# Kernel tuning notes

Measured on AMD Instinct MI355X. Metric: run time of the kernel, lower is better.

## Reference

```python
import jax, jax.numpy as jnp
import numpy as np

N, E = 50000, 800000
F_IN, HID, HEADS, OUT, NG = 128, 32, 4, 64, 64
HD = HID * HEADS  # 128


def gat_layer(x, src, dst, W, a_s, a_d, b, heads, out_c):
    n = x.shape[0]
    h = (x @ W).reshape(n, heads, out_c)                      # [N,H,C]
    al_s = jnp.einsum('nhc,hc->nh', h, a_s)                   # [N,H]
    al_d = jnp.einsum('nhc,hc->nh', h, a_d)
    e = jax.nn.leaky_relu(al_s[src] + al_d[dst], 0.2)         # [E,H]
    m = jax.ops.segment_max(e, dst, num_segments=n)
    ex = jnp.exp(e - m[dst])
    s = jax.ops.segment_sum(ex, dst, num_segments=n)
    alpha = ex / (s[dst] + 1e-16)                             # [E,H]
    msg = h[src] * alpha[:, :, None]                          # [E,H,C]
    out = jax.ops.segment_sum(msg, dst, num_segments=n)       # [N,H,C]
    return out.reshape(n, heads * out_c) + b


def batchnorm(x, g, be, eps=1e-5):
    mu = x.mean(0)
    var = x.var(0)
    return (x - mu) * jax.lax.rsqrt(var + eps) * g + be


def setup_inputs():
    key = jax.random.key(0)
    ks = jax.random.split(key, 32)
    inp = {}
    inp['x'] = jax.random.normal(ks[0], (N, F_IN), dtype=jnp.float32)
    inp['edge_index'] = jax.random.randint(ks[1], (2, E), 0, N, dtype=jnp.int64)
    inp['batch_ids'] = jnp.sort(jax.random.randint(ks[2], (N,), 0, NG, dtype=jnp.int64))
    dims = [(F_IN, HEADS, HID), (HD, HEADS, HID), (HD, HEADS, HID), (HD, 1, OUT)]
    for i, (din, h, c) in enumerate(dims):
        sc = 1.0 / np.sqrt(din)
        inp[f'W{i}'] = jax.random.normal(ks[3 + 4 * i], (din, h * c), dtype=jnp.float32) * sc
        inp[f'as{i}'] = jax.random.normal(ks[4 + 4 * i], (h, c), dtype=jnp.float32) * 0.1
        inp[f'ad{i}'] = jax.random.normal(ks[5 + 4 * i], (h, c), dtype=jnp.float32) * 0.1
        inp[f'b{i}'] = jnp.zeros((h * c,), dtype=jnp.float32)
    for i in range(3):
        inp[f'g{i}'] = jnp.ones((HD,), dtype=jnp.float32)
        inp[f'be{i}'] = jnp.zeros((HD,), dtype=jnp.float32)
    return inp


def reference(x, edge_index, batch_ids,
              W0, as0, ad0, b0, W1, as1, ad1, b1,
              W2, as2, ad2, b2, W3, as3, ad3, b3,
              g0, be0, g1, be1, g2, be2):
    # add self-loops (PyG GATConv default)
    loop = jnp.arange(N, dtype=edge_index.dtype)
    src = jnp.concatenate([edge_index[0], loop])
    dst = jnp.concatenate([edge_index[1], loop])

    h = x
    layers = [(W0, as0, ad0, b0, g0, be0), (W1, as1, ad1, b1, g1, be1),
              (W2, as2, ad2, b2, g2, be2)]
    for (W, a_s, a_d, b, g, be) in layers:
        h = gat_layer(h, src, dst, W, a_s, a_d, b, HEADS, HID)
        h = jax.nn.elu(batchnorm(h, g, be))
        # dropout p=0.6 is identity at inference
    h = gat_layer(h, src, dst, W3, as3, ad3, b3, 1, OUT)     # [N,OUT]

    # global mean pool over graphs
    ones = jnp.ones((N,), dtype=h.dtype)
    cnt = jax.ops.segment_sum(ones, batch_ids, num_segments=NG)
    summed = jax.ops.segment_sum(h, batch_ids, num_segments=NG)
    return summed / jnp.maximum(cnt, 1.0)[:, None]           # [NG,OUT]
```

## Files before the change

### kernel.cpp

```cpp
#include <hip/hip_runtime.h>

#define DEVINL __device__ __forceinline__

constexpr int N_NODES = 50000;
constexpr int E_EDGES = 800000;
constexpr int HD      = 128;
constexpr int NG      = 64;
constexpr int OUTC    = 64;
constexpr int NPAR    = 22;
constexpr int PAR_TOTAL = 3*(16384+3*128) + (8192+3*64) + 6*128;
constexpr int WT_TOTAL = 3*128*128 + 64*128;
constexpr int NB      = (N_NODES + 1023) / 1024;
constexpr int EBC     = 2048;
constexpr int NBLKC   = (E_EDGES + EBC - 1) / EBC;
constexpr int BNSLOTS = 16;

typedef _Float16 half8_t __attribute__((ext_vector_type(8)));
typedef _Float16 half4_t __attribute__((ext_vector_type(4)));
typedef float    float4_t __attribute__((ext_vector_type(4)));

DEVINL float bf2f(unsigned short u){
  union { unsigned int i; float f; } v; v.i = ((unsigned int)u) << 16; return v.f;
}
DEVINL float lrelu(float v){ return v > 0.f ? v : 0.2f * v; }

struct PtrTab { const void* p[NPAR]; int off[NPAR + 1]; };

__global__ void k_prep(PtrTab tab, const unsigned short* __restrict__ x,
                       const int* __restrict__ ei, int* __restrict__ flags,
                       float* __restrict__ dst,
                       const void* __restrict__ W0, const void* __restrict__ W1,
                       const void* __restrict__ W2, const void* __restrict__ W3,
                       _Float16* __restrict__ wt16){
  __shared__ int s_f32, s_i64;
  int t = threadIdx.x;
  if (t == 0){ s_f32 = 0; s_i64 = 1; }
  __syncthreads();
  for (int i = t; i < 2048; i += 256){
    float v = bf2f(x[i]);
    if (!(fabsf(v) < 1e4f)) s_f32 = 1;
  }
  for (int i = t; i < 512; i += 256){
    if (ei[2 * i + 1] != 0) s_i64 = 0;
  }
  __syncthreads();
  int f = s_f32;
  if (blockIdx.x == 0 && t == 0){ flags[0] = s_i64; flags[1] = s_f32; }

  int i = blockIdx.x * 256 + t;
  if (i < PAR_TOTAL){
    int k = 0;
    while (tab.off[k + 1] <= i) k++;
    int j = i - tab.off[k];
    dst[i] = f ? ((const float*)tab.p[k])[j] : bf2f(((const unsigned short*)tab.p[k])[j]);
    return;
  }
  int w = i - PAR_TOTAL;
  if (w >= WT_TOTAL) return;
  const void* W; int base, Mt;
  if (w < 49152){ int l = w >> 14; base = w & 16383; Mt = 128; W = (l == 0) ? W0 : (l == 1 ? W1 : W2); }
  else { base = w - 49152; Mt = 64; W = W3; }
  int nn = base >> 7, k = base & 127;
  float val = f ? ((const float*)W)[(size_t)k * Mt + nn]
                : bf2f(((const unsigned short*)W)[(size_t)k * Mt + nn]);
  wt16[w] = (_Float16)val;
}

__global__ __launch_bounds__(256) void k_count(const int* __restrict__ ei,
                      const int* __restrict__ flags, int* __restrict__ cntmat){
  __shared__ int cnt[NB];
  int t = threadIdx.x, blk = blockIdx.x;
  if (t < NB) cnt[t] = 0;
  __syncthreads();
  int f = flags[0];
  int e0 = blk * EBC;
  #pragma unroll
  for (int j = 0; j < EBC / 256; j++){
    int e = e0 + t + j * 256;
    if (e < E_EDGES){
      int d = ei[(size_t)(E_EDGES + e) << f];
      atomicAdd(&cnt[d >> 10], 1);
    }
  }
  __syncthreads();
  if (t < NB) cntmat[blk * NB + t] = cnt[t];
}

__global__ void k_scanmat(const int* __restrict__ cntmat, int* __restrict__ gbase,
                          int* __restrict__ bbase){
  __shared__ int cbase[NB + 1];
  __shared__ int csum[NB];
  int t = threadIdx.x;
  int s = 0;
  if (t < NB){
    for (int blk = 0; blk < NBLKC; blk++) s += cntmat[blk * NB + t];
    csum[t] = s;
  }
  __syncthreads();
  if (t == 0){
    int run = 0;
    for (int b = 0; b < NB; b++){ cbase[b] = run; run += csum[b]; }
    cbase[NB] = run;
  }
  __syncthreads();
  if (t <= NB) bbase[t] = cbase[t];
  if (t < NB){
    int run = cbase[t];
    for (int blk = 0; blk < NBLKC; blk++){
      gbase[blk * NB + t] = run;
      run += cntmat[blk * NB + t];
    }
  }
}

__global__ __launch_bounds__(256) void k_binscatter(const int* __restrict__ ei,
                      const int* __restrict__ flags, const int* __restrict__ gbase,
                      unsigned int* __restrict__ ebuf2){
  __shared__ int cur[NB];
  int t = threadIdx.x, blk = blockIdx.x;
  if (t < NB) cur[t] = gbase[blk * NB + t];
  __syncthreads();
  int f = flags[0];
  int e0 = blk * EBC;
  #pragma unroll
  for (int j = 0; j < EBC / 256; j++){
    int e = e0 + t + j * 256;
    if (e < E_EDGES){
      int s = ei[(size_t)e << f];
      int d = ei[(size_t)(E_EDGES + e) << f];
      int p = atomicAdd(&cur[d >> 10], 1);
      ebuf2[p] = (unsigned int)s | ((unsigned int)d << 16);
    }
  }
}

__global__ __launch_bounds__(256) void k_csrD(const unsigned int* __restrict__ ebuf2,
                      const int* __restrict__ bbase, int* __restrict__ offs,
                      int* __restrict__ ssrc, int n){
  __shared__ int hist[1024];
  __shared__ int wsum[256];
  int t = threadIdx.x, b = blockIdx.x;
  int nbase = b << 10;
  int s0 = bbase[b], s1 = bbase[b + 1];
  for (int i = t; i < 1024; i += 256) hist[i] = 0;
  __syncthreads();
  for (int i = s0 + t; i < s1; i += 256){
    unsigned int pk = ebuf2[i];
    atomicAdd(&hist[(int)(pk >> 16) - nbase], 1);
  }
  __syncthreads();
  int base4 = t * 4;
  int v0 = hist[base4], v1 = hist[base4 + 1], v2 = hist[base4 + 2], v3 = hist[base4 + 3];
  int s = v0 + v1 + v2 + v3;
  wsum[t] = s; __syncthreads();
  for (int off = 1; off < 256; off <<= 1){
    int x2 = (t >= off) ? wsum[t - off] : 0;
    __syncthreads();
    wsum[t] += x2;
    __syncthreads();
  }
  int run = s0 + wsum[t] - s;
  int node = nbase + base4;
  if (node < n) offs[node] = run;  hist[base4] = run;  run += v0;
  if (node + 1 < n) offs[node + 1] = run;  hist[base4 + 1] = run;  run += v1;
  if (node + 2 < n) offs[node + 2] = run;  hist[base4 + 2] = run;  run += v2;
  if (node + 3 < n) offs[node + 3] = run;  hist[base4 + 3] = run;
  if (b == NB - 1 && t == 255) offs[n] = s1;
  __syncthreads();
  for (int i = s0 + t; i < s1; i += 256){
    unsigned int pk = ebuf2[i];
    int p = atomicAdd(&hist[(int)(pk >> 16) - nbase], 1);
    ssrc[p] = (int)(pk & 0xFFFFu);
  }
}

template<int MT, bool FIRST>
__global__ __launch_bounds__(256) void k_gemm(
    const void* __restrict__ Ain, const int* __restrict__ flags,
    const float* __restrict__ bnslots,
    const float* __restrict__ g, const float* __restrict__ be,
    const _Float16* __restrict__ Wt16,
    const float* __restrict__ a_s, const float* __restrict__ a_d,
    _Float16* __restrict__ h16, float* __restrict__ als, float* __restrict__ ald,
    int n){
  __shared__ _Float16 AhL[64 * 136];
  __shared__ _Float16 WtL[MT * 72];
  __shared__ float scale[128], shift[128];
  const int t = threadIdx.x;
  const int rowBase = blockIdx.x * 64;
  if (!FIRST){
    if (t < 128){
      float s = 0.f, q = 0.f;
      #pragma unroll
      for (int sl = 0; sl < BNSLOTS; sl++){
        s += bnslots[sl * 256 + t];
        q += bnslots[sl * 256 + 128 + t];
      }
      float inv_n = 1.f / (float)n;
      float mu = s * inv_n;
      float var = q * inv_n - mu * mu;
      float sc = g[t] * rsqrtf(var + 1e-5f);
      scale[t] = sc; shift[t] = be[t] - mu * sc;
    }
    __syncthreads();
  }
  for (int f = t; f < 64 * 16; f += 256){
    int r = f >> 4, c8 = (f & 15) << 3;
    int row = rowBase + r;
    float v[8];
    if (row < n){
      if (FIRST){
        if (flags[1]){
          float4 x0 = *(const float4*)((const float*)Ain + (size_t)row * 128 + c8);
          float4 x1 = *(const float4*)((const float*)Ain + (size_t)row * 128 + c8 + 4);
          v[0]=x0.x; v[1]=x0.y; v[2]=x0.z; v[3]=x0.w;
          v[4]=x1.x; v[5]=x1.y; v[6]=x1.z; v[7]=x1.w;
        } else {
          const unsigned short* xp = (const unsigned short*)Ain + (size_t)row * 128 + c8;
          ushort4 u0 = *(const ushort4*)xp; ushort4 u1 = *(const ushort4*)(xp + 4);
          v[0]=bf2f(u0.x); v[1]=bf2f(u0.y); v[2]=bf2f(u0.z); v[3]=bf2f(u0.w);
          v[4]=bf2f(u1.x); v[5]=bf2f(u1.y); v[6]=bf2f(u1.z); v[7]=bf2f(u1.w);
        }
      } else {
        half8_t a8 = *(const half8_t*)((const _Float16*)Ain + (size_t)row * 128 + c8);
        #pragma unroll
        for (int j = 0; j < 8; j++){
          float xv = (float)a8[j] * scale[c8 + j] + shift[c8 + j];
          v[j] = xv > 0.f ? xv : (__expf(xv) - 1.f);
        }
      }
    } else {
      #pragma unroll
      for (int j = 0; j < 8; j++) v[j] = 0.f;
    }
    half8_t h;
    #pragma unroll
    for (int j = 0; j < 8; j++) h[j] = (_Float16)v[j];
    *(half8_t*)&AhL[r * 136 + c8] = h;
  }
  const int lane = t & 63;
  const int m = lane & 15, quad = lane >> 4;
  const int band = (t >> 6) * 16;
  float4_t acc[MT / 16];
  #pragma unroll
  for (int ct = 0; ct < MT / 16; ct++) acc[ct] = (float4_t){0.f, 0.f, 0.f, 0.f};
  #pragma unroll
  for (int kh = 0; kh < 2; kh++){
    __syncthreads();
    for (int f = t; f < MT * 8; f += 256){
      int nn = f >> 3, c8 = (f & 7) << 3;
      *(half8_t*)&WtL[nn * 72 + c8] = *(const half8_t*)&Wt16[nn * 128 + kh * 64 + c8];
    }
    __syncthreads();
    half8_t a0 = *(half8_t*)&AhL[(band + m) * 136 + kh * 64 + quad * 8];
    half8_t a1 = *(half8_t*)&AhL[(band + m) * 136 + kh * 64 + 32 + quad * 8];
    #pragma unroll
    for (int ct = 0; ct < MT / 16; ct++){
      half8_t b0 = *(half8_t*)&WtL[(ct * 16 + m) * 72 + quad * 8];
      half8_t b1 = *(half8_t*)&WtL[(ct * 16 + m) * 72 + 32 + quad * 8];
      acc[ct] = __builtin_amdgcn_mfma_f32_16x16x32_f16(a0, b0, acc[ct], 0, 0, 0);
      acc[ct] = __builtin_amdgcn_mfma_f32_16x16x32_f16(a1, b1, acc[ct], 0, 0, 0);
    }
  }
  __syncthreads();
  #pragma unroll
  for (int ct = 0; ct < MT / 16; ct++)
    #pragma unroll
    for (int rg = 0; rg < 4; rg++)
      AhL[(band + quad * 4 + rg) * 136 + ct * 16 + m] = (_Float16)acc[ct][rg];
  __syncthreads();
  int r = t >> 2, q = t & 3;
  int row = rowBase + r;
  if (MT == 128){
    if (row < n){
      half8_t h0 = *(half8_t*)&AhL[r * 136 + q * 32];
      half8_t h1 = *(half8_t*)&AhL[r * 136 + q * 32 + 8];
      half8_t h2 = *(half8_t*)&AhL[r * 136 + q * 32 + 16];
      half8_t h3 = *(half8_t*)&AhL[r * 136 + q * 32 + 24];
      float pas = 0.f, pad = 0.f;
      #pragma unroll
      for (int j = 0; j < 8; j++){
        pas += (float)h0[j] * a_s[q * 32 + j]      + (float)h1[j] * a_s[q * 32 + 8 + j]
             + (float)h2[j] * a_s[q * 32 + 16 + j] + (float)h3[j] * a_s[q * 32 + 24 + j];
        pad += (float)h0[j] * a_d[q * 32 + j]      + (float)h1[j] * a_d[q * 32 + 8 + j]
             + (float)h2[j] * a_d[q * 32 + 16 + j] + (float)h3[j] * a_d[q * 32 + 24 + j];
      }
      als[(size_t)row * 4 + q] = pas;
      ald[(size_t)row * 4 + q] = pad;
      _Float16* hp = h16 + (size_t)row * 128 + q * 32;
      *(half8_t*)hp = h0; *(half8_t*)(hp + 8) = h1;
      *(half8_t*)(hp + 16) = h2; *(half8_t*)(hp + 24) = h3;
    }
  } else {
    half8_t h0 = *(half8_t*)&AhL[r * 136 + q * 16];
    half8_t h1 = *(half8_t*)&AhL[r * 136 + q * 16 + 8];
    float pas = 0.f, pad = 0.f;
    #pragma unroll
    for (int j = 0; j < 8; j++){
      pas += (float)h0[j] * a_s[q * 16 + j] + (float)h1[j] * a_s[q * 16 + 8 + j];
      pad += (float)h0[j] * a_d[q * 16 + j] + (float)h1[j] * a_d[q * 16 + 8 + j];
    }
    pas += __shfl_xor(pas, 1); pas += __shfl_xor(pas, 2);
    pad += __shfl_xor(pad, 1); pad += __shfl_xor(pad, 2);
    if (row < n){
      _Float16* hp = h16 + (size_t)row * 64 + q * 16;
      *(half8_t*)hp = h0; *(half8_t*)(hp + 8) = h1;
      if (q == 0){ als[row] = pas; ald[row] = pad; }
    }
  }
}

template<int H, int C, int MODE>
__global__ __launch_bounds__(256) void k_attn(const _Float16* __restrict__ h16,
                      const float* __restrict__ als, const float* __restrict__ ald,
                      const int* __restrict__ offs, const int* __restrict__ ssrc,
                      const float* __restrict__ bias,
                      _Float16* __restrict__ a16out, float* __restrict__ bnout,
                      const int* __restrict__ bids, const int* __restrict__ flags,
                      float* __restrict__ psum, int* __restrict__ gcnt, int n){
  constexpr int HC = H * C;
  constexpr int CPL = HC / 16;
  int t = threadIdx.x;
  int nib  = t >> 4;
  int node = blockIdx.x * 16 + nib;
  int sub  = t & 15;
  int c0   = sub * CPL;
  int head = c0 / C;

  float ald_h = ald[(size_t)node * H + head];
  float acc[CPL];
  float ssum;
  {
    float w = __expf(lrelu(als[(size_t)node * H + head] + ald_h));
    ssum = w;
    const _Float16* hp = h16 + (size_t)node * HC + c0;
    #pragma unroll
    for (int i = 0; i < CPL; i++) acc[i] = w * (float)hp[i];
  }
  int beg = offs[node];
  int deg = offs[node + 1] - beg;
  int j = 0;
  for (; j + 8 <= deg; j += 8){
    int ss[8]; float al[8]; float w[8];
    #pragma unroll
    for (int u = 0; u < 8; u++) ss[u] = ssrc[beg + j + u];
    #pragma unroll
    for (int u = 0; u < 8; u++) al[u] = als[(size_t)ss[u] * H + head];
    if constexpr (CPL == 8){
      half8_t v[8];
      #pragma unroll
      for (int u = 0; u < 8; u++) v[u] = *(const half8_t*)(h16 + (size_t)ss[u] * HC + c0);
      #pragma unroll
      for (int u = 0; u < 8; u++){ w[u] = __expf(lrelu(al[u] + ald_h)); ssum += w[u]; }
      #pragma unroll
      for (int i = 0; i < 8; i++){
        float a = 0.f;
        #pragma unroll
        for (int u = 0; u < 8; u++) a += w[u] * (float)v[u][i];
        acc[i] += a;
      }
    } else {
      half4_t v[8];
      #pragma unroll
      for (int u = 0; u < 8; u++) v[u] = *(const half4_t*)(h16 + (size_t)ss[u] * HC + c0);
      #pragma unroll
      for (int u = 0; u < 8; u++){ w[u] = __expf(lrelu(al[u] + ald_h)); ssum += w[u]; }
      #pragma unroll
      for (int i = 0; i < 4; i++){
        float a = 0.f;
        #pragma unroll
        for (int u = 0; u < 8; u++) a += w[u] * (float)v[u][i];
        acc[i] += a;
      }
    }
  }
  for (; j + 4 <= deg; j += 4){
    int s0 = ssrc[beg + j], s1 = ssrc[beg + j + 1];
    int s2 = ssrc[beg + j + 2], s3 = ssrc[beg + j + 3];
    float al0 = als[(size_t)s0 * H + head], al1 = als[(size_t)s1 * H + head];
    float al2 = als[(size_t)s2 * H + head], al3 = als[(size_t)s3 * H + head];
    float w0 = __expf(lrelu(al0 + ald_h)), w1 = __expf(lrelu(al1 + ald_h));
    float w2 = __expf(lrelu(al2 + ald_h)), w3 = __expf(lrelu(al3 + ald_h));
    ssum += (w0 + w1) + (w2 + w3);
    if constexpr (CPL == 8){
      half8_t v0 = *(const half8_t*)(h16 + (size_t)s0 * HC + c0);
      half8_t v1 = *(const half8_t*)(h16 + (size_t)s1 * HC + c0);
      half8_t v2 = *(const half8_t*)(h16 + (size_t)s2 * HC + c0);
      half8_t v3 = *(const half8_t*)(h16 + (size_t)s3 * HC + c0);
      #pragma unroll
      for (int i = 0; i < 8; i++)
        acc[i] += w0 * (float)v0[i] + w1 * (float)v1[i]
                + w2 * (float)v2[i] + w3 * (float)v3[i];
    } else {
      half4_t v0 = *(const half4_t*)(h16 + (size_t)s0 * HC + c0);
      half4_t v1 = *(const half4_t*)(h16 + (size_t)s1 * HC + c0);
      half4_t v2 = *(const half4_t*)(h16 + (size_t)s2 * HC + c0);
      half4_t v3 = *(const half4_t*)(h16 + (size_t)s3 * HC + c0);
      #pragma unroll
      for (int i = 0; i < 4; i++)
        acc[i] += w0 * (float)v0[i] + w1 * (float)v1[i]
                + w2 * (float)v2[i] + w3 * (float)v3[i];
    }
  }
  for (; j < deg; j++){
    int s0 = ssrc[beg + j];
    float w0 = __expf(lrelu(als[(size_t)s0 * H + head] + ald_h));
    ssum += w0;
    const _Float16* hp = h16 + (size_t)s0 * HC + c0;
    #pragma unroll
    for (int i = 0; i < CPL; i++) acc[i] += w0 * (float)hp[i];
  }
  float inv_s = 1.f / ssum;
  float v[CPL];
  #pragma unroll
  for (int i = 0; i < CPL; i++) v[i] = acc[i] * inv_s + bias[c0 + i];

  if constexpr (MODE == 0){
    _Float16* op = a16out + (size_t)node * HC + c0;
    half8_t o;
    #pragma unroll
    for (int i = 0; i < CPL; i++) o[i] = (_Float16)v[i];
    *(half8_t*)op = o;
    __shared__ float red[16][132];
    *(float4*)&red[nib][c0]     = make_float4(v[0], v[1], v[2], v[3]);
    *(float4*)&red[nib][c0 + 4] = make_float4(v[4], v[5], v[6], v[7]);
    __syncthreads();
    if (t < 128){
      float s = 0.f, q = 0.f;
      #pragma unroll
      for (int i = 0; i < 16; i++){ float x = red[i][t]; s += x; q += x * x; }
      int slot = blockIdx.x & (BNSLOTS - 1);
      atomicAdd(&bnout[slot * 256 + t], s);
      atomicAdd(&bnout[slot * 256 + 128 + t], q);
    }
  } else {
    __shared__ float pacc[2][64];
    __shared__ int pcnt[2];
    int f = flags[0];
    if (t < 128) pacc[t >> 6][t & 63] = 0.f;
    if (t < 2) pcnt[t] = 0;
    __syncthreads();
    int g  = (int)bids[(size_t)node << f];
    int g0 = (int)bids[(size_t)(blockIdx.x * 16) << f];
    int g1 = (int)bids[(size_t)(blockIdx.x * 16 + 15) << f];
    if (g1 - g0 <= 1){
      int gl = g - g0;
      #pragma unroll
      for (int i = 0; i < 4; i++) atomicAdd(&pacc[gl][c0 + i], v[i]);
      if (sub == 0) atomicAdd(&pcnt[gl], 1);
      __syncthreads();
      if (t < 128){
        int gl2 = t >> 6;
        if (pcnt[gl2] > 0) atomicAdd(&psum[(g0 + gl2) * 64 + (t & 63)], pacc[gl2][t & 63]);
      }
      if (t < 2 && pcnt[t] > 0) atomicAdd(&gcnt[g0 + t], pcnt[t]);
    } else {
      #pragma unroll
      for (int i = 0; i < 4; i++) atomicAdd(&psum[g * 64 + c0 + i], v[i]);
      if (sub == 0) atomicAdd(&gcnt[g], 1);
      __syncthreads();
    }
  }
}

__global__ void k_pool_fin(const float* __restrict__ psum, const int* __restrict__ gcnt,
                           float* __restrict__ out){
  int i = blockIdx.x * 256 + threadIdx.x;
  if (i >= NG * OUTC) return;
  int cnt = gcnt[i >> 6];
  out[i] = psum[i] / (float)(cnt > 1 ? cnt : 1);
}

extern "C" void kernel_launch(void* const* d_in, const int* in_sizes, int n_in,
                              void* d_out, int out_size, void* d_ws, size_t ws_size,
                              hipStream_t stream){
  const unsigned short* x    = (const unsigned short*)d_in[0];
  const int*            ei   = (const int*)d_in[1];
  const int*            bids = (const int*)d_in[2];

  char* p = (char*)d_ws;
  auto carve = [&](size_t bytes) -> void* {
    void* r = (void*)p; p += (bytes + 255) & ~size_t(255); return r;
  };
  _Float16* a16    = (_Float16*)carve((size_t)N_NODES * HD * 2);
  _Float16* h16    = (_Float16*)carve((size_t)N_NODES * HD * 2);
  float*    par    = (float*)carve((size_t)PAR_TOTAL * 4);
  _Float16* wt16   = (_Float16*)carve((size_t)WT_TOTAL * 2);
  float*    als    = (float*)carve((size_t)N_NODES * 4 * 4);
  float*    ald    = (float*)carve((size_t)N_NODES * 4 * 4);
  int*      offs   = (int*)carve((size_t)(N_NODES + 1) * 4);
  int*      ssrc   = (int*)carve((size_t)E_EDGES * 4);
  unsigned int* ebuf2 = (unsigned int*)carve((size_t)E_EDGES * 4);
  int*      cntmat = (int*)carve((size_t)NBLKC * NB * 4);
  int*      gbase  = (int*)carve((size_t)NBLKC * NB * 4);
  int*      bbase  = (int*)carve((size_t)(NB + 1) * 4);
  int*      flags  = (int*)carve(256);
  char*     zbeg   = p;
  float*    bnbuf  = (float*)carve((size_t)3 * BNSLOTS * 256 * 4);
  float*    psum   = (float*)carve(NG * OUTC * 4);
  int*      gcnt   = (int*)carve(256);
  size_t    zlen   = (size_t)(p - zbeg);

  PtrTab tab;
  int sizes[NPAR];
  for (int l = 0; l < 4; l++){
    int base = 3 + 4 * l;
    tab.p[4 * l + 0] = d_in[base + 0]; sizes[4 * l + 0] = (l < 3) ? 16384 : 8192;
    tab.p[4 * l + 1] = d_in[base + 1]; sizes[4 * l + 1] = (l < 3) ? 128 : 64;
    tab.p[4 * l + 2] = d_in[base + 2]; sizes[4 * l + 2] = (l < 3) ? 128 : 64;
    tab.p[4 * l + 3] = d_in[base + 3]; sizes[4 * l + 3] = (l < 3) ? 128 : 64;
  }
  for (int l = 0; l < 3; l++){
    tab.p[16 + 2 * l]     = d_in[19 + 2 * l];     sizes[16 + 2 * l] = 128;
    tab.p[16 + 2 * l + 1] = d_in[19 + 2 * l + 1]; sizes[16 + 2 * l + 1] = 128;
  }
  tab.off[0] = 0;
  for (int k = 0; k < NPAR; k++) tab.off[k + 1] = tab.off[k] + sizes[k];
  const float* pAS[4], *pAD[4], *pB[4], *pG[3], *pBE[3];
  for (int l = 0; l < 4; l++){
    pAS[l] = par + tab.off[4 * l + 1];
    pAD[l] = par + tab.off[4 * l + 2];
    pB[l]  = par + tab.off[4 * l + 3];
  }
  for (int l = 0; l < 3; l++){
    pG[l]  = par + tab.off[16 + 2 * l];
    pBE[l] = par + tab.off[16 + 2 * l + 1];
  }
  const _Float16* pWT[4] = { wt16, wt16 + 16384, wt16 + 32768, wt16 + 49152 };
  float* bnS[3];
  for (int l = 0; l < 3; l++) bnS[l] = bnbuf + (size_t)l * BNSLOTS * 256;

  hipMemsetAsync(zbeg, 0, zlen, stream);

  k_prep<<<(PAR_TOTAL + WT_TOTAL + 255) / 256, 256, 0, stream>>>(
      tab, x, ei, flags, par, d_in[3], d_in[7], d_in[11], d_in[15], wt16);

  k_count<<<NBLKC, 256, 0, stream>>>(ei, flags, cntmat);
  k_scanmat<<<1, 256, 0, stream>>>(cntmat, gbase, bbase);
  k_binscatter<<<NBLKC, 256, 0, stream>>>(ei, flags, gbase, ebuf2);
  k_csrD<<<NB, 256, 0, stream>>>(ebuf2, bbase, offs, ssrc, N_NODES);

  int gemmBlocks = (N_NODES + 63) / 64;
  int attnBlocks = N_NODES / 16;

  k_gemm<128, true><<<gemmBlocks, 256, 0, stream>>>(
      (const void*)x, flags, nullptr, nullptr, nullptr,
      pWT[0], pAS[0], pAD[0], h16, als, ald, N_NODES);
  k_attn<4, 32, 0><<<attnBlocks, 256, 0, stream>>>(h16, als, ald, offs, ssrc, pB[0],
      a16, bnS[0], nullptr, nullptr, nullptr, nullptr, N_NODES);
  for (int l = 1; l < 3; l++){
    k_gemm<128, false><<<gemmBlocks, 256, 0, stream>>>(
        (const void*)a16, flags, bnS[l-1], pG[l-1], pBE[l-1],
        pWT[l], pAS[l], pAD[l], h16, als, ald, N_NODES);
    k_attn<4, 32, 0><<<attnBlocks, 256, 0, stream>>>(h16, als, ald, offs, ssrc, pB[l],
        a16, bnS[l], nullptr, nullptr, nullptr, nullptr, N_NODES);
  }
  k_gemm<64, false><<<gemmBlocks, 256, 0, stream>>>(
      (const void*)a16, flags, bnS[2], pG[2], pBE[2],
      pWT[3], pAS[3], pAD[3], h16, als, ald, N_NODES);
  k_attn<1, 64, 1><<<attnBlocks, 256, 0, stream>>>(h16, als, ald, offs, ssrc, pB[3],
      nullptr, nullptr, bids, flags, psum, gcnt, N_NODES);

  k_pool_fin<<<16, 256, 0, stream>>>(psum, gcnt, (float*)d_out);
}
```

Before: 437.1 us.

## Fuse CSR build kernels into one cooperative kernel with grid syncs

Merges the prep, count, scan, bin-scatter and CSR kernels into a single cooperative launch separated by grid-wide barriers. Packed edges are kept in registers between the count and scatter phases, so the edge list is read only once. The count matrix is transposed so that a parallel per-bin scan replaces the single-block serial scan. This removes several launch gaps and a second read of the edges, at the cost of grid.sync overhead and a hard requirement that all NBLKC blocks be co-resident.

New measurement: 632.9 us. 44.8% more time.

```diff
diff --git a/kernel.cpp b/kernel.cpp
--- a/kernel.cpp
+++ b/kernel.cpp
@@ -1,4 +1,7 @@
 #include <hip/hip_runtime.h>
+#include <hip/hip_cooperative_groups.h>
+
+namespace cg = cooperative_groups;
 
 #define DEVINL __device__ __forceinline__
 
@@ -26,14 +29,22 @@
 
 struct PtrTab { const void* p[NPAR]; int off[NPAR + 1]; };
 
-__global__ void k_prep(PtrTab tab, const unsigned short* __restrict__ x,
-                       const int* __restrict__ ei, int* __restrict__ flags,
-                       float* __restrict__ dst,
-                       const void* __restrict__ W0, const void* __restrict__ W1,
-                       const void* __restrict__ W2, const void* __restrict__ W3,
-                       _Float16* __restrict__ wt16){
+__global__ __launch_bounds__(256) void k_build(PtrTab tab,
+    const unsigned short* __restrict__ x, const int* __restrict__ ei,
+    int* __restrict__ flags, float* __restrict__ par,
+    const void* __restrict__ W0, const void* __restrict__ W1,
+    const void* __restrict__ W2, const void* __restrict__ W3,
+    _Float16* __restrict__ wt16,
+    int* __restrict__ cntmat,
+    int* __restrict__ gbase,
+    int* __restrict__ csum_g,
+    int* __restrict__ cbase,
+    unsigned int* __restrict__ ebuf2,
+    int* __restrict__ offs, int* __restrict__ ssrc){
+  cg::grid_group grid = cg::this_grid();
+  int t = threadIdx.x, blk = blockIdx.x;
+
   __shared__ int s_f32, s_i64;
-  int t = threadIdx.x;
   if (t == 0){ s_f32 = 0; s_i64 = 1; }
   __syncthreads();
   for (int i = t; i < 2048; i += 256){
@@ -44,133 +55,120 @@
     if (ei[2 * i + 1] != 0) s_i64 = 0;
   }
   __syncthreads();
-  int f = s_f32;
-  if (blockIdx.x == 0 && t == 0){ flags[0] = s_i64; flags[1] = s_f32; }
-
-  int i = blockIdx.x * 256 + t;
-  if (i < PAR_TOTAL){
-    int k = 0;
-    while (tab.off[k + 1] <= i) k++;
-    int j = i - tab.off[k];
-    dst[i] = f ? ((const float*)tab.p[k])[j] : bf2f(((const unsigned short*)tab.p[k])[j]);
-    return;
-  }
-  int w = i - PAR_TOTAL;
-  if (w >= WT_TOTAL) return;
-  const void* W; int base, Mt;
-  if (w < 49152){ int l = w >> 14; base = w & 16383; Mt = 128; W = (l == 0) ? W0 : (l == 1 ? W1 : W2); }
-  else { base = w - 49152; Mt = 64; W = W3; }
-  int nn = base >> 7, k = base & 127;
-  float val = f ? ((const float*)W)[(size_t)k * Mt + nn]
-                : bf2f(((const unsigned short*)W)[(size_t)k * Mt + nn]);
-  wt16[w] = (_Float16)val;
-}
-
-__global__ __launch_bounds__(256) void k_count(const int* __restrict__ ei,
-                      const int* __restrict__ flags, int* __restrict__ cntmat){
+  const int f32 = s_f32, i64 = s_i64;
+  if (blk == 0 && t == 0){ flags[0] = i64; flags[1] = f32; }
+
+  for (int i = blk * 256 + t; i < PAR_TOTAL + WT_TOTAL; i += gridDim.x * 256){
+    if (i < PAR_TOTAL){
+      int k = 0;
+      while (tab.off[k + 1] <= i) k++;
+      int j = i - tab.off[k];
+      par[i] = f32 ? ((const float*)tab.p[k])[j] : bf2f(((const unsigned short*)tab.p[k])[j]);
+    } else {
+      int w = i - PAR_TOTAL;
+      const void* W; int base, Mt;
+      if (w < 49152){ int l = w >> 14; base = w & 16383; Mt = 128; W = (l == 0) ? W0 : (l == 1 ? W1 : W2); }
+      else { base = w - 49152; Mt = 64; W = W3; }
+      int nn = base >> 7, k = base & 127;
+      float val = f32 ? ((const float*)W)[(size_t)k * Mt + nn]
+                      : bf2f(((const unsigned short*)W)[(size_t)k * Mt + nn]);
+      wt16[w] = (_Float16)val;
+    }
+  }
+
+  unsigned int my[EBC / 256];
   __shared__ int cnt[NB];
-  int t = threadIdx.x, blk = blockIdx.x;
-  if (t < NB) cnt[t] = 0;
-  __syncthreads();
-  int f = flags[0];
-  int e0 = blk * EBC;
-  #pragma unroll
-  for (int j = 0; j < EBC / 256; j++){
-    int e = e0 + t + j * 256;
-    if (e < E_EDGES){
-      int d = ei[(size_t)(E_EDGES + e) << f];
-      atomicAdd(&cnt[d >> 10], 1);
-    }
-  }
-  __syncthreads();
-  if (t < NB) cntmat[blk * NB + t] = cnt[t];
-}
-
-__global__ void k_scanmat(const int* __restrict__ cntmat, int* __restrict__ gbase,
-                          int* __restrict__ bbase){
-  __shared__ int cbase[NB + 1];
-  __shared__ int csum[NB];
-  int t = threadIdx.x;
-  int s = 0;
-  if (t < NB){
-    for (int blk = 0; blk < NBLKC; blk++) s += cntmat[blk * NB + t];
-    csum[t] = s;
-  }
-  __syncthreads();
-  if (t == 0){
+  if (blk < NBLKC){
+    if (t < NB) cnt[t] = 0;
+    __syncthreads();
+    int e0 = blk * EBC;
+    #pragma unroll
+    for (int j = 0; j < EBC / 256; j++){
+      int e = e0 + t + j * 256;
+      my[j] = 0xFFFFFFFFu;
+      if (e < E_EDGES){
+        int s = ei[(size_t)e << i64];
+        int d = ei[(size_t)(E_EDGES + e) << i64];
+        my[j] = (unsigned int)s | ((unsigned int)d << 16);
+        atomicAdd(&cnt[d >> 10], 1);
+      }
+    }
+    __syncthreads();
+    if (t < NB) cntmat[t * NBLKC + blk] = cnt[t];
+  }
+  grid.sync();
+
+  __shared__ int vals[NBLKC];
+  if (blk < NB){
+    for (int k = t; k < NBLKC; k += 256) vals[k] = cntmat[blk * NBLKC + k];
+    __syncthreads();
+    if (t == 0){
+      int run = 0;
+      for (int k = 0; k < NBLKC; k++){ int c = vals[k]; vals[k] = run; run += c; }
+      csum_g[blk] = run;
+    }
+    __syncthreads();
+    for (int k = t; k < NBLKC; k += 256) gbase[blk * NBLKC + k] = vals[k];
+  }
+  grid.sync();
+
+  if (blk == 0 && t == 0){
     int run = 0;
-    for (int b = 0; b < NB; b++){ cbase[b] = run; run += csum[b]; }
+    for (int b = 0; b < NB; b++){ cbase[b] = run; run += csum_g[b]; }
     cbase[NB] = run;
   }
-  __syncthreads();
-  if (t <= NB) bbase[t] = cbase[t];
-  if (t < NB){
-    int run = cbase[t];
-    for (int blk = 0; blk < NBLKC; blk++){
-      gbase[blk * NB + t] = run;
-      run += cntmat[blk * NB + t];
-    }
-  }
-}
-
-__global__ __launch_bounds__(256) void k_binscatter(const int* __restrict__ ei,
-                      const int* __restrict__ flags, const int* __restrict__ gbase,
-                      unsigned int* __restrict__ ebuf2){
+  grid.sync();
+
   __shared__ int cur[NB];
-  int t = threadIdx.x, blk = blockIdx.x;
-  if (t < NB) cur[t] = gbase[blk * NB + t];
-  __syncthreads();
-  int f = flags[0];
-  int e0 = blk * EBC;
-  #pragma unroll
-  for (int j = 0; j < EBC / 256; j++){
-    int e = e0 + t + j * 256;
-    if (e < E_EDGES){
-      int s = ei[(size_t)e << f];
-      int d = ei[(size_t)(E_EDGES + e) << f];
-      int p = atomicAdd(&cur[d >> 10], 1);
-      ebuf2[p] = (unsigned int)s | ((unsigned int)d << 16);
-    }
-  }
-}
-
-__global__ __launch_bounds__(256) void k_csrD(const unsigned int* __restrict__ ebuf2,
-                      const int* __restrict__ bbase, int* __restrict__ offs,
-                      int* __restrict__ ssrc, int n){
+  if (blk < NBLKC){
+    if (t < NB) cur[t] = gbase[t * NBLKC + blk] + cbase[t];
+    __syncthreads();
+    #pragma unroll
+    for (int j = 0; j < EBC / 256; j++){
+      unsigned int pk = my[j];
+      if (pk != 0xFFFFFFFFu){
+        int p = atomicAdd(&cur[pk >> 26], 1);
+        ebuf2[p] = pk;
+      }
+    }
+  }
+  grid.sync();
+
   __shared__ int hist[1024];
   __shared__ int wsum[256];
-  int t = threadIdx.x, b = blockIdx.x;
-  int nbase = b << 10;
-  int s0 = bbase[b], s1 = bbase[b + 1];
-  for (int i = t; i < 1024; i += 256) hist[i] = 0;
-  __syncthreads();
-  for (int i = s0 + t; i < s1; i += 256){
-    unsigned int pk = ebuf2[i];
-    atomicAdd(&hist[(int)(pk >> 16) - nbase], 1);
-  }
-  __syncthreads();
-  int base4 = t * 4;
-  int v0 = hist[base4], v1 = hist[base4 + 1], v2 = hist[base4 + 2], v3 = hist[base4 + 3];
-  int s = v0 + v1 + v2 + v3;
-  wsum[t] = s; __syncthreads();
-  for (int off = 1; off < 256; off <<= 1){
-    int x2 = (t >= off) ? wsum[t - off] : 0;
-    __syncthreads();
-    wsum[t] += x2;
-    __syncthreads();
-  }
-  int run = s0 + wsum[t] - s;
-  int node = nbase + base4;
-  if (node < n) offs[node] = run;  hist[base4] = run;  run += v0;
-  if (node + 1 < n) offs[node + 1] = run;  hist[base4 + 1] = run;  run += v1;
-  if (node + 2 < n) offs[node + 2] = run;  hist[base4 + 2] = run;  run += v2;
-  if (node + 3 < n) offs[node + 3] = run;  hist[base4 + 3] = run;
-  if (b == NB - 1 && t == 255) offs[n] = s1;
-  __syncthreads();
-  for (int i = s0 + t; i < s1; i += 256){
-    unsigned int pk = ebuf2[i];
-    int p = atomicAdd(&hist[(int)(pk >> 16) - nbase], 1);
-    ssrc[p] = (int)(pk & 0xFFFFu);
+  if (blk < NB){
+    int nbase = blk << 10;
+    int s0 = cbase[blk], s1 = cbase[blk + 1];
+    for (int i = t; i < 1024; i += 256) hist[i] = 0;
+    __syncthreads();
+    for (int i = s0 + t; i < s1; i += 256){
+      unsigned int pk = ebuf2[i];
+      atomicAdd(&hist[(int)(pk >> 16) - nbase], 1);
+    }
+    __syncthreads();
+    int base4 = t * 4;
+    int v0 = hist[base4], v1 = hist[base4 + 1], v2 = hist[base4 + 2], v3 = hist[base4 + 3];
+    int s = v0 + v1 + v2 + v3;
+    wsum[t] = s; __syncthreads();
+    for (int off = 1; off < 256; off <<= 1){
+      int x2 = (t >= off) ? wsum[t - off] : 0;
+      __syncthreads();
+      wsum[t] += x2;
+      __syncthreads();
+    }
+    int run = s0 + wsum[t] - s;
+    int node = nbase + base4;
+    if (node < N_NODES) offs[node] = run;  hist[base4] = run;  run += v0;
+    if (node + 1 < N_NODES) offs[node + 1] = run;  hist[base4 + 1] = run;  run += v1;
+    if (node + 2 < N_NODES) offs[node + 2] = run;  hist[base4 + 2] = run;  run += v2;
+    if (node + 3 < N_NODES) offs[node + 3] = run;  hist[base4 + 3] = run;
+    if (blk == NB - 1 && t == 255) offs[N_NODES] = s1;
+    __syncthreads();
+    for (int i = s0 + t; i < s1; i += 256){
+      unsigned int pk = ebuf2[i];
+      int p = atomicAdd(&hist[(int)(pk >> 16) - nbase], 1);
+      ssrc[p] = (int)(pk & 0xFFFFu);
+    }
   }
 }
 
@@ -491,9 +489,10 @@
   int*      offs   = (int*)carve((size_t)(N_NODES + 1) * 4);
   int*      ssrc   = (int*)carve((size_t)E_EDGES * 4);
   unsigned int* ebuf2 = (unsigned int*)carve((size_t)E_EDGES * 4);
-  int*      cntmat = (int*)carve((size_t)NBLKC * NB * 4);
-  int*      gbase  = (int*)carve((size_t)NBLKC * NB * 4);
-  int*      bbase  = (int*)carve((size_t)(NB + 1) * 4);
+  int*      cntmat = (int*)carve((size_t)NB * NBLKC * 4);
+  int*      gbase  = (int*)carve((size_t)NB * NBLKC * 4);
+  int*      csum_g = (int*)carve(256);
+  int*      cbase  = (int*)carve((size_t)(NB + 1) * 4);
   int*      flags  = (int*)carve(256);
   char*     zbeg   = p;
   float*    bnbuf  = (float*)carve((size_t)3 * BNSLOTS * 256 * 4);
@@ -532,13 +531,12 @@
 
   hipMemsetAsync(zbeg, 0, zlen, stream);
 
-  k_prep<<<(PAR_TOTAL + WT_TOTAL + 255) / 256, 256, 0, stream>>>(
-      tab, x, ei, flags, par, d_in[3], d_in[7], d_in[11], d_in[15], wt16);
-
-  k_count<<<NBLKC, 256, 0, stream>>>(ei, flags, cntmat);
-  k_scanmat<<<1, 256, 0, stream>>>(cntmat, gbase, bbase);
-  k_binscatter<<<NBLKC, 256, 0, stream>>>(ei, flags, gbase, ebuf2);
-  k_csrD<<<NB, 256, 0, stream>>>(ebuf2, bbase, offs, ssrc, N_NODES);
+  const void* W0 = d_in[3], *W1 = d_in[7], *W2 = d_in[11], *W3 = d_in[15];
+  void* args[] = { (void*)&tab, (void*)&x, (void*)&ei, (void*)&flags, (void*)&par,
+                   (void*)&W0, (void*)&W1, (void*)&W2, (void*)&W3, (void*)&wt16,
+                   (void*)&cntmat, (void*)&gbase, (void*)&csum_g, (void*)&cbase,
+                   (void*)&ebuf2, (void*)&offs, (void*)&ssrc };
+  hipLaunchCooperativeKernel((void*)k_build, dim3(NBLKC), dim3(256), args, 0, stream);
 
   int gemmBlocks = (N_NODES + 63) / 64;
   int attnBlocks = N_NODES / 16;
```

## Replace per-block count matrix scan with global atomic bin totals and cursors

Applied to the files above, without the earlier changes.

The per-block bin count matrix and its serial single-block scan are replaced by global atomic per-bin totals, a tiny prefix kernel, and atomic cursor reservation inside the scatter kernel. This removes the sequential loop over about 400 blocks per bin in the scan kernel, which was a serial bottleneck. The scatter kernel now keeps packed edges in registers and does a local histogram before reserving global ranges, so edge order within a bin becomes nondeterministic. The CSR build kernel sorts by destination within each bin, so correctness is preserved, though source order per node may vary.

Result: faster. 422.9 us (-3.2%).

```diff
diff --git a/kernel.cpp b/kernel.cpp
--- a/kernel.cpp
+++ b/kernel.cpp
@@ -67,7 +67,7 @@
 }
 
 __global__ __launch_bounds__(256) void k_count(const int* __restrict__ ei,
-                      const int* __restrict__ flags, int* __restrict__ cntmat){
+                      const int* __restrict__ flags, int* __restrict__ btot){
   __shared__ int cnt[NB];
   int t = threadIdx.x, blk = blockIdx.x;
   if (t < NB) cnt[t] = 0;
@@ -83,65 +83,66 @@
     }
   }
   __syncthreads();
-  if (t < NB) cntmat[blk * NB + t] = cnt[t];
-}
-
-__global__ void k_scanmat(const int* __restrict__ cntmat, int* __restrict__ gbase,
-                          int* __restrict__ bbase){
-  __shared__ int cbase[NB + 1];
-  __shared__ int csum[NB];
+  if (t < NB && cnt[t] > 0) atomicAdd(&btot[t], cnt[t]);
+}
+
+__global__ void k_cbase(const int* __restrict__ btot, int* __restrict__ cbase,
+                        int* __restrict__ cursor){
   int t = threadIdx.x;
-  int s = 0;
-  if (t < NB){
-    for (int blk = 0; blk < NBLKC; blk++) s += cntmat[blk * NB + t];
-    csum[t] = s;
-  }
-  __syncthreads();
+  __shared__ int cb[NB + 1];
   if (t == 0){
     int run = 0;
-    for (int b = 0; b < NB; b++){ cbase[b] = run; run += csum[b]; }
-    cbase[NB] = run;
-  }
-  __syncthreads();
-  if (t <= NB) bbase[t] = cbase[t];
-  if (t < NB){
-    int run = cbase[t];
-    for (int blk = 0; blk < NBLKC; blk++){
-      gbase[blk * NB + t] = run;
-      run += cntmat[blk * NB + t];
-    }
-  }
+    for (int b = 0; b < NB; b++){ cb[b] = run; run += btot[b]; }
+    cb[NB] = run;
+  }
+  __syncthreads();
+  if (t <= NB) cbase[t] = cb[t];
+  if (t < NB)  cursor[t] = cb[t];
 }
 
 __global__ __launch_bounds__(256) void k_binscatter(const int* __restrict__ ei,
-                      const int* __restrict__ flags, const int* __restrict__ gbase,
+                      const int* __restrict__ flags, int* __restrict__ cursor,
                       unsigned int* __restrict__ ebuf2){
+  __shared__ int cnt[NB];
   __shared__ int cur[NB];
   int t = threadIdx.x, blk = blockIdx.x;
-  if (t < NB) cur[t] = gbase[blk * NB + t];
+  if (t < NB) cnt[t] = 0;
   __syncthreads();
   int f = flags[0];
   int e0 = blk * EBC;
+  unsigned int my[EBC / 256];
   #pragma unroll
   for (int j = 0; j < EBC / 256; j++){
     int e = e0 + t + j * 256;
+    my[j] = 0xFFFFFFFFu;
     if (e < E_EDGES){
       int s = ei[(size_t)e << f];
       int d = ei[(size_t)(E_EDGES + e) << f];
-      int p = atomicAdd(&cur[d >> 10], 1);
-      ebuf2[p] = (unsigned int)s | ((unsigned int)d << 16);
+      my[j] = (unsigned int)s | ((unsigned int)d << 16);
+      atomicAdd(&cnt[d >> 10], 1);
+    }
+  }
+  __syncthreads();
+  if (t < NB && cnt[t] > 0) cur[t] = atomicAdd(&cursor[t], cnt[t]);
+  __syncthreads();
+  #pragma unroll
+  for (int j = 0; j < EBC / 256; j++){
+    unsigned int pk = my[j];
+    if (pk != 0xFFFFFFFFu){
+      int p = atomicAdd(&cur[pk >> 26], 1);
+      ebuf2[p] = pk;
     }
   }
 }
 
 __global__ __launch_bounds__(256) void k_csrD(const unsigned int* __restrict__ ebuf2,
-                      const int* __restrict__ bbase, int* __restrict__ offs,
+                      const int* __restrict__ cbase, int* __restrict__ offs,
                       int* __restrict__ ssrc, int n){
   __shared__ int hist[1024];
   __shared__ int wsum[256];
   int t = threadIdx.x, b = blockIdx.x;
   int nbase = b << 10;
-  int s0 = bbase[b], s1 = bbase[b + 1];
+  int s0 = cbase[b], s1 = cbase[b + 1];
   for (int i = t; i < 1024; i += 256) hist[i] = 0;
   __syncthreads();
   for (int i = s0 + t; i < s1; i += 256){
@@ -491,11 +492,11 @@
   int*      offs   = (int*)carve((size_t)(N_NODES + 1) * 4);
   int*      ssrc   = (int*)carve((size_t)E_EDGES * 4);
   unsigned int* ebuf2 = (unsigned int*)carve((size_t)E_EDGES * 4);
-  int*      cntmat = (int*)carve((size_t)NBLKC * NB * 4);
-  int*      gbase  = (int*)carve((size_t)NBLKC * NB * 4);
-  int*      bbase  = (int*)carve((size_t)(NB + 1) * 4);
+  int*      cbase  = (int*)carve((size_t)(NB + 1) * 4);
+  int*      cursor = (int*)carve(256);
   int*      flags  = (int*)carve(256);
   char*     zbeg   = p;
+  int*      btot   = (int*)carve(256);
   float*    bnbuf  = (float*)carve((size_t)3 * BNSLOTS * 256 * 4);
   float*    psum   = (float*)carve(NG * OUTC * 4);
   int*      gcnt   = (int*)carve(256);
@@ -535,10 +536,10 @@
   k_prep<<<(PAR_TOTAL + WT_TOTAL + 255) / 256, 256, 0, stream>>>(
       tab, x, ei, flags, par, d_in[3], d_in[7], d_in[11], d_in[15], wt16);
 
-  k_count<<<NBLKC, 256, 0, stream>>>(ei, flags, cntmat);
-  k_scanmat<<<1, 256, 0, stream>>>(cntmat, gbase, bbase);
-  k_binscatter<<<NBLKC, 256, 0, stream>>>(ei, flags, gbase, ebuf2);
-  k_csrD<<<NB, 256, 0, stream>>>(ebuf2, bbase, offs, ssrc, N_NODES);
+  k_count<<<NBLKC, 256, 0, stream>>>(ei, flags, btot);
+  k_cbase<<<1, 64, 0, stream>>>(btot, cbase, cursor);
+  k_binscatter<<<NBLKC, 256, 0, stream>>>(ei, flags, cursor, ebuf2);
+  k_csrD<<<NB, 256, 0, stream>>>(ebuf2, cbase, offs, ssrc, N_NODES);
 
   int gemmBlocks = (N_NODES + 63) / 64;
   int attnBlocks = N_NODES / 16;
```
